# Kernel tuning notes

Measured on AMD Instinct MI355X. Metric: run time of the kernel, lower is better.

## Reference

```python
import jax, jax.numpy as jnp
import numpy as np

B, H, S, DK, DV = 4, 16, 2048, 64, 64

def setup_inputs() -> dict:
    key = jax.random.key(0)
    k1, k2, k3, k4 = jax.random.split(key, 4)
    Q = jax.random.normal(k1, (B, H, S, DK), dtype=jnp.float32)
    K = jax.random.normal(k2, (B, H, S, DK), dtype=jnp.float32)
    V = jax.random.normal(k3, (B, H, S, DV), dtype=jnp.float32)
    mask_out = jax.random.randint(k4, (B, 1, 1, S), 0, 2).astype(jnp.bool_)
    return {"Q": Q, "K": K, "V": V, "mask_out": mask_out}

def reference(Q, K, V, mask_out):
    key_size = Q.shape[-1]
    seq_q, seq_k = Q.shape[-2], K.shape[-2]
    scale = jnp.sqrt(jnp.float32(key_size))
    # scores: [B, H, Sq, Sk]
    scores = jnp.einsum('bhqd,bhkd->bhqk', Q, K) / scale
    scores = jnp.where(mask_out, jnp.float32(-1e9), scores)
    attn = jax.nn.softmax(scores, axis=-1)
    # Gaussian relative-position decay: exp(-|i-j|^2 / (Sk^2 / 2))
    idx_q = jnp.arange(seq_q, dtype=jnp.float32)[:, None]
    idx_k = jnp.arange(seq_k, dtype=jnp.float32)[None, :]
    rel = idx_q - idx_k  # [Sq, Sk]
    decay = jnp.exp(-(rel * rel) * (2.0 / (seq_k * seq_k)))  # [Sq, Sk]
    attn = attn * decay  # broadcast over [B, H]
    return jnp.einsum('bhqk,bhkv->bhqv', attn, V)
```

## Files before the change

kernel.cpp:

```cpp
#include <hip/hip_runtime.h>
#include <hip/hip_bf16.h>
#include <hip/hip_fp16.h>

typedef __attribute__((ext_vector_type(8))) short bf16x8;
typedef __attribute__((ext_vector_type(4))) short bf16x4;
typedef __attribute__((ext_vector_type(4))) float f32x4;
typedef __attribute__((ext_vector_type(4))) unsigned u32x4;
typedef __attribute__((ext_vector_type(4))) int i32x4;

constexpr int Bn = 4, Hn = 16, S = 2048, D = 64;
constexpr int BQ = 128;
constexpr float LOG2E = 1.44269504088896340736f;

__device__ __forceinline__ unsigned cvtpk(float lo, float hi) {
    unsigned r;
    asm("v_cvt_pk_bf16_f32 %0, %1, %2" : "=v"(r) : "v"(lo), "v"(hi));
    return r;
}

__device__ __forceinline__ f32x4 mfma16(bf16x4 a, bf16x4 b, f32x4 c) {
#if __has_builtin(__builtin_amdgcn_mfma_f32_16x16x16bf16_1k)
    return __builtin_amdgcn_mfma_f32_16x16x16bf16_1k(a, b, c, 0, 0, 0);
#else
    asm volatile("v_mfma_f32_16x16x16_bf16 %0, %1, %2, %0"
                 : "+v"(c) : "v"(a), "v"(b));
    return c;
#endif
}

__device__ __forceinline__ void gload16(const short* g, short* lds) {
    __builtin_amdgcn_global_load_lds(
        (const __attribute__((address_space(1))) unsigned*)g,
        (__attribute__((address_space(3))) unsigned*)lds,
        16, 0, 0);
}

__global__ void compact_mask(const void* __restrict__ maskg,
                             int* __restrict__ idxp, int* __restrict__ Mg) {
    const int b = blockIdx.x, t = threadIdx.x;
    __shared__ int wsum[4];
    __shared__ int Msh;

    const unsigned* mu = (const unsigned*)maskg;
    bool is_bytes = false;
    #pragma unroll 8
    for (int i = 0; i < 64; ++i) is_bytes |= (mu[i] > 1u);

    int keep[8]; int cnt = 0;
    #pragma unroll
    for (int i = 0; i < 8; ++i) {
        const int key = t * 8 + i;
        int m;
        if (is_bytes) m = ((const unsigned char*)maskg)[b * S + key];
        else          m = ((const int*)maskg)[b * S + key];
        keep[i] = (m == 0);
        cnt += keep[i];
    }
    const int l = t & 63, w = t >> 6;
    int pre = cnt;
    #pragma unroll
    for (int d = 1; d < 64; d <<= 1) {
        int v = __shfl_up(pre, d, 64);
        if (l >= d) pre += v;
    }
    if (l == 63) wsum[w] = pre;
    __syncthreads();
    int base = 0;
    for (int i = 0; i < w; ++i) base += wsum[i];
    int offs = base + pre - cnt;
    #pragma unroll
    for (int i = 0; i < 8; ++i)
        if (keep[i]) idxp[b * S + (offs++)] = t * 8 + i;
    if (t == 255) Msh = base + pre;
    __syncthreads();
    const int M = Msh;
    for (int i = M + t; i < S; i += 256) idxp[b * S + i] = 0;
    if (M == 0)
        for (int i = t; i < S; i += 256) idxp[b * S + i] = i;
    if (t == 0) Mg[b] = (M == 0) ? -1 : M;
}

__global__ void pack_kv(const float* __restrict__ Kg, const float* __restrict__ Vg,
                        const int* __restrict__ idxp, const int* __restrict__ Mg,
                        short* __restrict__ Kw, short* __restrict__ Vw) {
    const int bh = blockIdx.x, b = bh >> 4;
    const int ck0 = blockIdx.y * 256;
    const int t = threadIdx.x;
    const int Mraw = Mg[b];
    const int M = (Mraw < 0) ? S : Mraw;
    if (ck0 >= M) return;
    const int* idxb = idxp + b * S;
    const float* Kp = Kg + (size_t)bh * S * D;
    const float* Vp = Vg + (size_t)bh * S * D;

    {
        const int dc = (t & 7) * 8;
        #pragma unroll
        for (int tile = 0; tile < 4; ++tile)
            #pragma unroll
            for (int it = 0; it < 2; ++it) {
                const int key = ck0 + tile * 64 + (t >> 3) + it * 32;
                u32x4 pk = u32x4{0u, 0u, 0u, 0u};
                if (key < M) {
                    const float* src = Kp + (size_t)idxb[key] * D + dc;
                    #pragma unroll
                    for (int jj = 0; jj < 4; ++jj)
                        pk[jj] = cvtpk(src[2 * jj], src[2 * jj + 1]);
                }
                *(u32x4*)(Kw + ((size_t)bh * S + key) * D + dc) = pk;
            }
    }
    {
        const int dv = t & 63;
        const int kb = (t >> 6) * 16;
        #pragma unroll
        for (int tile = 0; tile < 4; ++tile) {
            const int tg = (ck0 >> 6) + tile;
            float f[16];
            #pragma unroll
            for (int i = 0; i < 16; ++i) {
                const int key = ck0 + tile * 64 + kb + i;
                float v = 0.f;
                if (key < M) {
                    int row = idxb[key];
                    row = __builtin_amdgcn_readfirstlane(row);
                    v = Vp[(size_t)row * D + dv];
                }
                f[i] = v;
            }
            u32x4 p0, p1;
            #pragma unroll
            for (int jj = 0; jj < 4; ++jj) {
                p0[jj] = cvtpk(f[2 * jj], f[2 * jj + 1]);
                p1[jj] = cvtpk(f[8 + 2 * jj], f[9 + 2 * jj]);
            }
            short* dst = Vw + (((size_t)bh * 32 + tg) * 64 + dv) * 64 + kb;
            *(u32x4*)dst = p0;
            *(u32x4*)(dst + 8) = p1;
        }
    }
}

template<int MINW>
__global__ __launch_bounds__(512, MINW) void attn_packed(
    const float* __restrict__ Qg, const short* __restrict__ Kw,
    const short* __restrict__ Vw, const int* __restrict__ idxp,
    const int* __restrict__ Mg, float* __restrict__ outg)
{
    __shared__ alignas(16) short Kt[2][64][64];
    __shared__ alignas(16) short Vt[2][64][64];
    __shared__ alignas(16) __half dtab[2176];

    const int bid  = blockIdx.x;
    const int lblk = ((bid & 7) << 7) | (bid >> 3);
    const int qt   = lblk & 15;
    const int bh   = lblk >> 4;
    const int b    = bh >> 4;
    const int q0   = qt * BQ;

    const float* Qp   = Qg + ((size_t)bh * S + q0) * D;
    const short* Ksrc = Kw + (size_t)bh * S * D;
    const short* Vsrc = Vw + (size_t)bh * 32 * 64 * 64;
    float*       Op   = outg + ((size_t)bh * S + q0) * D;
    const int*   idxb = idxp + b * S;

    const int t  = threadIdx.x;
    const int w  = t >> 6;
    const int lr = t & 15;
    const int lg = (t & 63) >> 4;
    const int lx = lr & 7;

    const int  Mraw    = Mg[b];
    const bool uniform = (Mraw < 0);
    const int  M       = uniform ? S : Mraw;
    const int  ntiles  = (M + 63) >> 6;

    const int srcoff = ((t >> 3) << 6) + (((t & 7) ^ ((t >> 3) & 7)) << 3);
    const int wbase  = w << 9;

    gload16(Ksrc + srcoff, &Kt[0][0][0] + wbase);
    gload16(Vsrc + srcoff, &Vt[0][0][0] + wbase);

    const float CD2 = (2.0f / ((float)S * (float)S)) * LOG2E;
    for (int i = t; i < 2176; i += 512) {
        const float r = (float)(q0 + i - 2047);
        dtab[i] = __float2half(__builtin_exp2f(-CD2 * r * r));
    }

    const float qscale = uniform ? 0.0f : 0.125f * LOG2E;
    bf16x8 qf[2];
    {
        const int row = w * 16 + lr;
        #pragma unroll
        for (int g = 0; g < 2; ++g) {
            const float* src = Qp + row * D + g * 32 + lg * 8;
            union { unsigned u[4]; bf16x8 v; } cv;
            #pragma unroll
            for (int jj = 0; jj < 4; ++jj)
                cv.u[jj] = cvtpk(src[2 * jj] * qscale, src[2 * jj + 1] * qscale);
            qf[g] = cv.v;
        }
    }

    f32x4 Oacc[4];
    #pragma unroll
    for (int dt = 0; dt < 4; ++dt) Oacc[dt] = f32x4{0.f, 0.f, 0.f, 0.f};
    float lrun = 0.f;

    const int qi = w * 16 + lr + 2047;

    asm volatile("s_waitcnt vmcnt(0)" ::: "memory");
    __syncthreads();

    int c = 0;
    for (int tt = 0; tt < ntiles; ++tt) {
        const int  rem  = M - tt * 64;
        const bool last = (rem <= 64);

        if (tt + 1 < ntiles) {
            const size_t toff = (size_t)(tt + 1) * 4096 + srcoff;
            gload16(Ksrc + toff, &Kt[c ^ 1][0][0] + wbase);
            gload16(Vsrc + toff, &Vt[c ^ 1][0][0] + wbase);
        }

        const char* kbase = (const char*)&Kt[c][0][0];
        const char* vbase = (const char*)&Vt[c][0][0];

        float lp = 0.f;
        #pragma unroll
        for (int kt = 0; kt < 4; ++kt) {
            const bf16x8 kf0 = *(const bf16x8*)(kbase + (kt * 16 + lr) * 128
                                                + ((lg ^ lx) << 4));
            const bf16x8 kf1 = *(const bf16x8*)(kbase + (kt * 16 + lr) * 128
                                                + (((4 + lg) ^ lx) << 4));
            f32x4 s = f32x4{0.f, 0.f, 0.f, 0.f};
            __builtin_amdgcn_s_setprio(1);
            s = __builtin_amdgcn_mfma_f32_16x16x32_bf16(kf0, qf[0], s, 0, 0, 0);
            s = __builtin_amdgcn_mfma_f32_16x16x32_bf16(kf1, qf[1], s, 0, 0, 0);
            __builtin_amdgcn_s_setprio(0);

            const i32x4 iv = *(const i32x4*)(idxb + tt * 64 + kt * 16 + lg * 4);
            float p0 = __builtin_exp2f(s[0] - 16.0f);
            float p1 = __builtin_exp2f(s[1] - 16.0f);
            float p2 = __builtin_exp2f(s[2] - 16.0f);
            float p3 = __builtin_exp2f(s[3] - 16.0f);
            if (last) {
                const int ck = kt * 16 + lg * 4;
                p0 = (ck + 0 < rem) ? p0 : 0.f;
                p1 = (ck + 1 < rem) ? p1 : 0.f;
                p2 = (ck + 2 < rem) ? p2 : 0.f;
                p3 = (ck + 3 < rem) ? p3 : 0.f;
            }
            lp += (p0 + p1) + (p2 + p3);
            const float d0 = __half2float(dtab[qi - iv[0]]);
            const float d1 = __half2float(dtab[qi - iv[1]]);
            const float d2 = __half2float(dtab[qi - iv[2]]);
            const float d3 = __half2float(dtab[qi - iv[3]]);
            union { unsigned u[2]; bf16x4 v; } cx;
            cx.u[0] = cvtpk(p0 * d0, p1 * d1);
            cx.u[1] = cvtpk(p2 * d2, p3 * d3);
            const bf16x4 Xb = cx.v;

            __builtin_amdgcn_s_setprio(1);
            #pragma unroll
            for (int dt = 0; dt < 4; ++dt) {
                const bf16x4 vA = *(const bf16x4*)(vbase + (dt * 16 + lr) * 128
                          + ((((2 * kt + (lg >> 1)) ^ lx) << 4) | ((lg & 1) << 3)));
                Oacc[dt] = mfma16(vA, Xb, Oacc[dt]);
            }
            __builtin_amdgcn_s_setprio(0);
        }
        lrun += lp;

        asm volatile("s_waitcnt vmcnt(0)" ::: "memory");
        __syncthreads();
        c ^= 1;
    }

    {
        float ls = lrun;
        ls += __shfl_xor(ls, 16, 64);
        ls += __shfl_xor(ls, 32, 64);
        const float inv = 1.0f / ls;
        const int row = w * 16 + lr;
        #pragma unroll
        for (int dt = 0; dt < 4; ++dt) {
            f32x4 o = Oacc[dt];
            o[0] *= inv; o[1] *= inv; o[2] *= inv; o[3] *= inv;
            *(f32x4*)&Op[(size_t)row * D + dt * 16 + lg * 4] = o;
        }
    }
}

__global__ __launch_bounds__(256, 3) void attn_gather(
    const float* __restrict__ Qg, const float* __restrict__ Kg,
    const float* __restrict__ Vg, const int* __restrict__ idxp,
    const int* __restrict__ Mg, float* __restrict__ outg)
{
    __shared__ alignas(16) short Kt[64][72];
    __shared__ alignas(16) short Vt[64][72];
    __shared__ alignas(16) float dtab[2176];
    __shared__ alignas(16) int   idxs[64];

    const int blk = blockIdx.x;
    const int qt  = blk & 15;
    const int bh  = blk >> 4;
    const int b   = bh >> 4;
    const int q0  = qt * BQ;

    const float* Qp = Qg + ((size_t)bh * S + q0) * D;
    const float* Kp = Kg + (size_t)bh * S * D;
    const float* Vp = Vg + (size_t)bh * S * D;
    float*       Op = outg + ((size_t)bh * S + q0) * D;
    const int*   idxb = idxp + b * S;

    const int t  = threadIdx.x;
    const int w  = t >> 6;
    const int l  = t & 63;
    const int lr = l & 15;
    const int lg = l >> 4;

    const int  Mraw    = Mg[b];
    const bool uniform = (Mraw < 0);
    const int  M       = uniform ? S : Mraw;

    const float CD2 = (2.0f / ((float)S * (float)S)) * LOG2E;
    for (int i = t; i < 2176; i += 256) {
        const float r = (float)(q0 + i - 2047);
        dtab[i] = __builtin_exp2f(-CD2 * r * r);
    }

    const float qscale = uniform ? 0.0f : 0.125f * LOG2E;
    bf16x8 qf[2][2];
    #pragma unroll
    for (int rt = 0; rt < 2; ++rt) {
        const int row = w * 32 + rt * 16 + lr;
        #pragma unroll
        for (int g = 0; g < 2; ++g) {
            const float* src = Qp + row * D + g * 32 + lg * 8;
            union { unsigned u[4]; bf16x8 v; } cv;
            #pragma unroll
            for (int jj = 0; jj < 4; ++jj)
                cv.u[jj] = cvtpk(src[2 * jj] * qscale, src[2 * jj + 1] * qscale);
            qf[rt][g] = cv.v;
        }
    }

    f32x4 Oacc[2][4];
    #pragma unroll
    for (int rt = 0; rt < 2; ++rt)
        #pragma unroll
        for (int dt = 0; dt < 4; ++dt) Oacc[rt][dt] = f32x4{0.f, 0.f, 0.f, 0.f};
    float lrun[2] = {0.f, 0.f};

    const int qrl2047 = w * 32 + lr + 2047;

    for (int kv = 0; kv < M; kv += 64) {
        const int  rem  = M - kv;
        const bool last = (rem <= 64);
        __syncthreads();
        {
            const int key = t >> 3;
            const int dc  = (t & 7) * 8;
            #pragma unroll
            for (int it = 0; it < 2; ++it) {
                const int row = idxb[kv + key + it * 32];
                const float* src = Kp + (size_t)row * D + dc;
                u32x4 pk;
                #pragma unroll
                for (int jj = 0; jj < 4; ++jj)
                    pk[jj] = cvtpk(src[2 * jj], src[2 * jj + 1]);
                *(u32x4*)&Kt[key + it * 32][dc] = pk;
            }
        }
        if (t < 64) idxs[t] = idxb[kv + t];
        {
            const int dv = t & 63;
            const int kb = (t >> 6) * 16;
            float f[16];
            #pragma unroll
            for (int i = 0; i < 16; ++i) {
                int row = idxb[kv + kb + i];
                row = __builtin_amdgcn_readfirstlane(row);
                f[i] = Vp[(size_t)row * D + dv];
            }
            u32x4 p0, p1;
            #pragma unroll
            for (int jj = 0; jj < 4; ++jj) {
                p0[jj] = cvtpk(f[2 * jj], f[2 * jj + 1]);
                p1[jj] = cvtpk(f[8 + 2 * jj], f[9 + 2 * jj]);
            }
            *(u32x4*)&Vt[dv][kb]     = p0;
            *(u32x4*)&Vt[dv][kb + 8] = p1;
        }
        __syncthreads();

        bf16x8 kf[4][2];
        #pragma unroll
        for (int kt = 0; kt < 4; ++kt)
            #pragma unroll
            for (int g = 0; g < 2; ++g)
                kf[kt][g] = *(const bf16x8*)&Kt[kt * 16 + lr][g * 32 + lg * 8];

        bf16x4 Xb[2][4];
        #pragma unroll
        for (int rt = 0; rt < 2; ++rt) {
            f32x4 sc[4];
            #pragma unroll
            for (int kt = 0; kt < 4; ++kt) {
                f32x4 acc = f32x4{0.f, 0.f, 0.f, 0.f};
                acc = __builtin_amdgcn_mfma_f32_16x16x32_bf16(kf[kt][0], qf[rt][0], acc, 0, 0, 0);
                acc = __builtin_amdgcn_mfma_f32_16x16x32_bf16(kf[kt][1], qf[rt][1], acc, 0, 0, 0);
                sc[kt] = acc;
            }
            const int qi = qrl2047 + rt * 16;
            float lp = 0.f;
            #pragma unroll
            for (int kt = 0; kt < 4; ++kt) {
                const i32x4 iv = *(const i32x4*)&idxs[kt * 16 + lg * 4];
                float p0 = __builtin_exp2f(sc[kt][0] - 16.0f);
                float p1 = __builtin_exp2f(sc[kt][1] - 16.0f);
                float p2 = __builtin_exp2f(sc[kt][2] - 16.0f);
                float p3 = __builtin_exp2f(sc[kt][3] - 16.0f);
                if (last) {
                    const int ck = kt * 16 + lg * 4;
                    p0 = (ck + 0 < rem) ? p0 : 0.f;
                    p1 = (ck + 1 < rem) ? p1 : 0.f;
                    p2 = (ck + 2 < rem) ? p2 : 0.f;
                    p3 = (ck + 3 < rem) ? p3 : 0.f;
                }
                lp += (p0 + p1) + (p2 + p3);
                const float d0 = dtab[qi - iv[0]];
                const float d1 = dtab[qi - iv[1]];
                const float d2 = dtab[qi - iv[2]];
                const float d3 = dtab[qi - iv[3]];
                union { unsigned u[2]; bf16x4 v; } cx;
                cx.u[0] = cvtpk(p0 * d0, p1 * d1);
                cx.u[1] = cvtpk(p2 * d2, p3 * d3);
                Xb[rt][kt] = cx.v;
            }
            lrun[rt] += lp;
        }

        #pragma unroll
        for (int kt = 0; kt < 4; ++kt) {
            bf16x4 vA[4];
            #pragma unroll
            for (int dt = 0; dt < 4; ++dt)
                vA[dt] = *(const bf16x4*)&Vt[dt * 16 + lr][kt * 16 + lg * 4];
            #pragma unroll
            for (int dt = 0; dt < 4; ++dt) {
                Oacc[0][dt] = mfma16(vA[dt], Xb[0][kt], Oacc[0][dt]);
                Oacc[1][dt] = mfma16(vA[dt], Xb[1][kt], Oacc[1][dt]);
            }
        }
    }

    #pragma unroll
    for (int rt = 0; rt < 2; ++rt) {
        float ls = lrun[rt];
        ls += __shfl_xor(ls, 16, 64);
        ls += __shfl_xor(ls, 32, 64);
        const float inv = 1.0f / ls;
        const int row = w * 32 + rt * 16 + lr;
        #pragma unroll
        for (int dt = 0; dt < 4; ++dt) {
            f32x4 o = Oacc[rt][dt];
            o[0] *= inv; o[1] *= inv; o[2] *= inv; o[3] *= inv;
            *(f32x4*)&Op[(size_t)row * D + dt * 16 + lg * 4] = o;
        }
    }
}

extern "C" void kernel_launch(void* const* d_in, const int* in_sizes, int n_in,
                              void* d_out, int out_size, void* d_ws, size_t ws_size,
                              hipStream_t stream) {
    const float* Q = (const float*)d_in[0];
    const float* K = (const float*)d_in[1];
    const float* V = (const float*)d_in[2];
    const void*  M = d_in[3];
    float* out = (float*)d_out;

    int* idxp = (int*)d_ws;
    int* Mg   = idxp + Bn * S;
    size_t base = (((size_t)(Bn * S + Bn) * 4) + 255) & ~(size_t)255;
    short* Kw = (short*)((char*)d_ws + base);
    short* Vw = Kw + (size_t)Bn * Hn * S * D;
    const size_t need = base + 2 * (size_t)Bn * Hn * S * D * sizeof(short);

    compact_mask<<<dim3(Bn), dim3(256), 0, stream>>>(M, idxp, Mg);
    const int nblk = Bn * Hn * (S / BQ);
    if (ws_size >= need) {
        pack_kv<<<dim3(Bn * Hn, S / 256), dim3(256), 0, stream>>>(K, V, idxp, Mg, Kw, Vw);
        hipFuncAttributes fa8{};
        bool use8 = (hipFuncGetAttributes(&fa8,
                        reinterpret_cast<const void*>(&attn_packed<8>)) == hipSuccess)
                    && (fa8.localSizeBytes == 0);
        if (use8)
            attn_packed<8><<<dim3(nblk), dim3(512), 0, stream>>>(Q, Kw, Vw, idxp, Mg, out);
        else
            attn_packed<4><<<dim3(nblk), dim3(512), 0, stream>>>(Q, Kw, Vw, idxp, Mg, out);
    } else {
        attn_gather<<<dim3(nblk), dim3(256), 0, stream>>>(Q, K, V, idxp, Mg, out);
    }
}
```

Measured before the change: 120.7 us.

## Compute Gaussian decay analytically in exponent and process two row tiles per wave

Replaces the per-block half-precision decay lookup table and per-key index gathers with precomputed per-key exponent coefficients (e, f), so the decay folds into the softmax exp2 argument via an FMA. The coefficients are written by compact_mask and streamed into LDS alongside K/V tiles. The attention kernel drops to 256 threads, with each wave handling 32 query rows (two 16-row tiles) so every K/V LDS fragment is reused across both tiles. This doubles the exp2 count per score (one for the normaliser, one for the decayed weight) and raises register pressure, in exchange for removing the dtab build, the table lookups and the idx loads.

```diff
diff --git a/kernel.cpp b/kernel.cpp
--- a/kernel.cpp
+++ b/kernel.cpp
@@ -1,6 +1,5 @@
 #include <hip/hip_runtime.h>
 #include <hip/hip_bf16.h>
-#include <hip/hip_fp16.h>
 
 typedef __attribute__((ext_vector_type(8))) short bf16x8;
 typedef __attribute__((ext_vector_type(4))) short bf16x4;
@@ -11,6 +10,7 @@
 constexpr int Bn = 4, Hn = 16, S = 2048, D = 64;
 constexpr int BQ = 128;
 constexpr float LOG2E = 1.44269504088896340736f;
+constexpr float CD2f = (2.0f / ((float)S * (float)S)) * LOG2E;
 
 __device__ __forceinline__ unsigned cvtpk(float lo, float hi) {
     unsigned r;
@@ -36,7 +36,8 @@
 }
 
 __global__ void compact_mask(const void* __restrict__ maskg,
-                             int* __restrict__ idxp, int* __restrict__ Mg) {
+                             int* __restrict__ idxp, int* __restrict__ Mg,
+                             float* __restrict__ EFw) {
     const int b = blockIdx.x, t = threadIdx.x;
     __shared__ int wsum[4];
     __shared__ int Msh;
@@ -78,6 +79,19 @@
     if (M == 0)
         for (int i = t; i < S; i += 256) idxp[b * S + i] = i;
     if (t == 0) Mg[b] = (M == 0) ? -1 : M;
+
+    const int Meff = (M == 0) ? S : M;
+    for (int key = t; key < S; key += 256) {
+        float e = 0.f, f = 0.f;
+        if (key < Meff) {
+            const int j = (M == 0) ? key : idxp[b * S + key];
+            const float jf = (float)j;
+            f = 2.0f * CD2f * jf;
+            e = -CD2f * jf * jf;
+        }
+        float* dst = EFw + (size_t)b * 8192 + ((key >> 6) * 256 + (key & 63) * 2);
+        dst[0] = e; dst[1] = f;
+    }
 }
 
 __global__ void pack_kv(const float* __restrict__ Kg, const float* __restrict__ Vg,
@@ -141,15 +155,14 @@
     }
 }
 
-template<int MINW>
-__global__ __launch_bounds__(512, MINW) void attn_packed(
+__global__ __launch_bounds__(256, 4) void attn_packed(
     const float* __restrict__ Qg, const short* __restrict__ Kw,
-    const short* __restrict__ Vw, const int* __restrict__ idxp,
+    const short* __restrict__ Vw, const float* __restrict__ EFw,
     const int* __restrict__ Mg, float* __restrict__ outg)
 {
     __shared__ alignas(16) short Kt[2][64][64];
     __shared__ alignas(16) short Vt[2][64][64];
-    __shared__ alignas(16) __half dtab[2176];
+    __shared__ alignas(16) float EFt[2][256];
 
     const int bid  = blockIdx.x;
     const int lblk = ((bid & 7) << 7) | (bid >> 3);
@@ -158,16 +171,17 @@
     const int b    = bh >> 4;
     const int q0   = qt * BQ;
 
-    const float* Qp   = Qg + ((size_t)bh * S + q0) * D;
-    const short* Ksrc = Kw + (size_t)bh * S * D;
-    const short* Vsrc = Vw + (size_t)bh * 32 * 64 * 64;
-    float*       Op   = outg + ((size_t)bh * S + q0) * D;
-    const int*   idxb = idxp + b * S;
+    const float* Qp    = Qg + ((size_t)bh * S + q0) * D;
+    const short* Ksrc  = Kw + (size_t)bh * S * D;
+    const short* Vsrc  = Vw + (size_t)bh * 32 * 64 * 64;
+    const float* EFsrc = EFw + (size_t)b * 8192;
+    float*       Op    = outg + ((size_t)bh * S + q0) * D;
 
     const int t  = threadIdx.x;
     const int w  = t >> 6;
-    const int lr = t & 15;
-    const int lg = (t & 63) >> 4;
+    const int l  = t & 63;
+    const int lr = l & 15;
+    const int lg = l >> 4;
     const int lx = lr & 7;
 
     const int  Mraw    = Mg[b];
@@ -175,22 +189,28 @@
     const int  M       = uniform ? S : Mraw;
     const int  ntiles  = (M + 63) >> 6;
 
-    const int srcoff = ((t >> 3) << 6) + (((t & 7) ^ ((t >> 3) & 7)) << 3);
-    const int wbase  = w << 9;
-
-    gload16(Ksrc + srcoff, &Kt[0][0][0] + wbase);
-    gload16(Vsrc + srcoff, &Vt[0][0][0] + wbase);
-
-    const float CD2 = (2.0f / ((float)S * (float)S)) * LOG2E;
-    for (int i = t; i < 2176; i += 512) {
-        const float r = (float)(q0 + i - 2047);
-        dtab[i] = __float2half(__builtin_exp2f(-CD2 * r * r));
+    int so[2], ld[2];
+    #pragma unroll
+    for (int p = 0; p < 2; ++p) {
+        const int r = (p * 4 + w) * 8 + (l >> 3);
+        so[p] = r * 64 + (((l & 7) ^ (r & 7)) << 3);
+        ld[p] = (p * 4 + w) * 512;
+    }
+    const short* efl = (const short*)EFsrc + l * 8;
+
+    {
+        gload16(Ksrc + so[0], &Kt[0][0][0] + ld[0]);
+        gload16(Ksrc + so[1], &Kt[0][0][0] + ld[1]);
+        gload16(Vsrc + so[0], &Vt[0][0][0] + ld[0]);
+        gload16(Vsrc + so[1], &Vt[0][0][0] + ld[1]);
+        if (w == 0) gload16(efl, (short*)&EFt[0][0]);
     }
 
     const float qscale = uniform ? 0.0f : 0.125f * LOG2E;
-    bf16x8 qf[2];
-    {
-        const int row = w * 16 + lr;
+    bf16x8 qf[2][2];
+    #pragma unroll
+    for (int rt = 0; rt < 2; ++rt) {
+        const int row = w * 32 + rt * 16 + lr;
         #pragma unroll
         for (int g = 0; g < 2; ++g) {
             const float* src = Qp + row * D + g * 32 + lg * 8;
@@ -198,16 +218,24 @@
             #pragma unroll
             for (int jj = 0; jj < 4; ++jj)
                 cv.u[jj] = cvtpk(src[2 * jj] * qscale, src[2 * jj + 1] * qscale);
-            qf[g] = cv.v;
-        }
-    }
-
-    f32x4 Oacc[4];
-    #pragma unroll
-    for (int dt = 0; dt < 4; ++dt) Oacc[dt] = f32x4{0.f, 0.f, 0.f, 0.f};
-    float lrun = 0.f;
-
-    const int qi = w * 16 + lr + 2047;
+            qf[rt][g] = cv.v;
+        }
+    }
+
+    float if_[2], ci2[2];
+    #pragma unroll
+    for (int rt = 0; rt < 2; ++rt) {
+        const float iq = (float)(q0 + w * 32 + rt * 16 + lr);
+        if_[rt] = iq;
+        ci2[rt] = -CD2f * iq * iq;
+    }
+
+    f32x4 Oacc[2][4];
+    #pragma unroll
+    for (int rt = 0; rt < 2; ++rt)
+        #pragma unroll
+        for (int dt = 0; dt < 4; ++dt) Oacc[rt][dt] = f32x4{0.f, 0.f, 0.f, 0.f};
+    float lrun[2] = {0.f, 0.f};
 
     asm volatile("s_waitcnt vmcnt(0)" ::: "memory");
     __syncthreads();
@@ -218,74 +246,92 @@
         const bool last = (rem <= 64);
 
         if (tt + 1 < ntiles) {
-            const size_t toff = (size_t)(tt + 1) * 4096 + srcoff;
-            gload16(Ksrc + toff, &Kt[c ^ 1][0][0] + wbase);
-            gload16(Vsrc + toff, &Vt[c ^ 1][0][0] + wbase);
-        }
-
-        const char* kbase = (const char*)&Kt[c][0][0];
-        const char* vbase = (const char*)&Vt[c][0][0];
-
-        float lp = 0.f;
+            const short* kp = Ksrc + (size_t)(tt + 1) * 4096;
+            const short* vp = Vsrc + (size_t)(tt + 1) * 4096;
+            gload16(kp + so[0], &Kt[c ^ 1][0][0] + ld[0]);
+            gload16(kp + so[1], &Kt[c ^ 1][0][0] + ld[1]);
+            gload16(vp + so[0], &Vt[c ^ 1][0][0] + ld[0]);
+            gload16(vp + so[1], &Vt[c ^ 1][0][0] + ld[1]);
+            if (w == 0) gload16(efl + (size_t)(tt + 1) * 512, (short*)&EFt[c ^ 1][0]);
+        }
+
+        const char*  kbase = (const char*)&Kt[c][0][0];
+        const char*  vbase = (const char*)&Vt[c][0][0];
+        const float* efb   = &EFt[c][0];
+
         #pragma unroll
         for (int kt = 0; kt < 4; ++kt) {
             const bf16x8 kf0 = *(const bf16x8*)(kbase + (kt * 16 + lr) * 128
                                                 + ((lg ^ lx) << 4));
             const bf16x8 kf1 = *(const bf16x8*)(kbase + (kt * 16 + lr) * 128
                                                 + (((4 + lg) ^ lx) << 4));
-            f32x4 s = f32x4{0.f, 0.f, 0.f, 0.f};
+            f32x4 s0 = f32x4{0.f, 0.f, 0.f, 0.f};
+            f32x4 s1 = f32x4{0.f, 0.f, 0.f, 0.f};
             __builtin_amdgcn_s_setprio(1);
-            s = __builtin_amdgcn_mfma_f32_16x16x32_bf16(kf0, qf[0], s, 0, 0, 0);
-            s = __builtin_amdgcn_mfma_f32_16x16x32_bf16(kf1, qf[1], s, 0, 0, 0);
+            s0 = __builtin_amdgcn_mfma_f32_16x16x32_bf16(kf0, qf[0][0], s0, 0, 0, 0);
+            s0 = __builtin_amdgcn_mfma_f32_16x16x32_bf16(kf1, qf[0][1], s0, 0, 0, 0);
+            s1 = __builtin_amdgcn_mfma_f32_16x16x32_bf16(kf0, qf[1][0], s1, 0, 0, 0);
+            s1 = __builtin_amdgcn_mfma_f32_16x16x32_bf16(kf1, qf[1][1], s1, 0, 0, 0);
             __builtin_amdgcn_s_setprio(0);
 
-            const i32x4 iv = *(const i32x4*)(idxb + tt * 64 + kt * 16 + lg * 4);
-            float p0 = __builtin_exp2f(s[0] - 16.0f);
-            float p1 = __builtin_exp2f(s[1] - 16.0f);
-            float p2 = __builtin_exp2f(s[2] - 16.0f);
-            float p3 = __builtin_exp2f(s[3] - 16.0f);
-            if (last) {
-                const int ck = kt * 16 + lg * 4;
-                p0 = (ck + 0 < rem) ? p0 : 0.f;
-                p1 = (ck + 1 < rem) ? p1 : 0.f;
-                p2 = (ck + 2 < rem) ? p2 : 0.f;
-                p3 = (ck + 3 < rem) ? p3 : 0.f;
-            }
-            lp += (p0 + p1) + (p2 + p3);
-            const float d0 = __half2float(dtab[qi - iv[0]]);
-            const float d1 = __half2float(dtab[qi - iv[1]]);
-            const float d2 = __half2float(dtab[qi - iv[2]]);
-            const float d3 = __half2float(dtab[qi - iv[3]]);
-            union { unsigned u[2]; bf16x4 v; } cx;
-            cx.u[0] = cvtpk(p0 * d0, p1 * d1);
-            cx.u[1] = cvtpk(p2 * d2, p3 * d3);
-            const bf16x4 Xb = cx.v;
+            const f32x4 efA = *(const f32x4*)(efb + (kt * 16 + lg * 4) * 2);
+            const f32x4 efB = *(const f32x4*)(efb + (kt * 16 + lg * 4) * 2 + 4);
+
+            bf16x4 Xb[2];
+            #pragma unroll
+            for (int rt = 0; rt < 2; ++rt) {
+                const f32x4 s = rt ? s1 : s0;
+                const float iq = if_[rt], cc = ci2[rt];
+                const float u0 = fmaf(efA[1], iq, efA[0]) + cc;
+                const float u1 = fmaf(efA[3], iq, efA[2]) + cc;
+                const float u2 = fmaf(efB[1], iq, efB[0]) + cc;
+                const float u3 = fmaf(efB[3], iq, efB[2]) + cc;
+                const float a0 = s[0] - 16.0f, a1 = s[1] - 16.0f;
+                const float a2 = s[2] - 16.0f, a3 = s[3] - 16.0f;
+                float p0 = __builtin_exp2f(a0), q0_ = __builtin_exp2f(a0 + u0);
+                float p1 = __builtin_exp2f(a1), q1_ = __builtin_exp2f(a1 + u1);
+                float p2 = __builtin_exp2f(a2), q2_ = __builtin_exp2f(a2 + u2);
+                float p3 = __builtin_exp2f(a3), q3_ = __builtin_exp2f(a3 + u3);
+                if (last) {
+                    const int ck = kt * 16 + lg * 4;
+                    p0 = (ck + 0 < rem) ? p0 : 0.f;  q0_ = (ck + 0 < rem) ? q0_ : 0.f;
+                    p1 = (ck + 1 < rem) ? p1 : 0.f;  q1_ = (ck + 1 < rem) ? q1_ : 0.f;
+                    p2 = (ck + 2 < rem) ? p2 : 0.f;  q2_ = (ck + 2 < rem) ? q2_ : 0.f;
+                    p3 = (ck + 3 < rem) ? p3 : 0.f;  q3_ = (ck + 3 < rem) ? q3_ : 0.f;
+                }
+                lrun[rt] += (p0 + p1) + (p2 + p3);
+                union { unsigned u[2]; bf16x4 v; } cx;
+                cx.u[0] = cvtpk(q0_, q1_);
+                cx.u[1] = cvtpk(q2_, q3_);
+                Xb[rt] = cx.v;
+            }
 
             __builtin_amdgcn_s_setprio(1);
             #pragma unroll
             for (int dt = 0; dt < 4; ++dt) {
                 const bf16x4 vA = *(const bf16x4*)(vbase + (dt * 16 + lr) * 128
                           + ((((2 * kt + (lg >> 1)) ^ lx) << 4) | ((lg & 1) << 3)));
-                Oacc[dt] = mfma16(vA, Xb, Oacc[dt]);
+                Oacc[0][dt] = mfma16(vA, Xb[0], Oacc[0][dt]);
+                Oacc[1][dt] = mfma16(vA, Xb[1], Oacc[1][dt]);
             }
             __builtin_amdgcn_s_setprio(0);
         }
-        lrun += lp;
 
         asm volatile("s_waitcnt vmcnt(0)" ::: "memory");
         __syncthreads();
         c ^= 1;
     }
 
-    {
-        float ls = lrun;
+    #pragma unroll
+    for (int rt = 0; rt < 2; ++rt) {
+        float ls = lrun[rt];
         ls += __shfl_xor(ls, 16, 64);
         ls += __shfl_xor(ls, 32, 64);
         const float inv = 1.0f / ls;
-        const int row = w * 16 + lr;
+        const int row = w * 32 + rt * 16 + lr;
         #pragma unroll
         for (int dt = 0; dt < 4; ++dt) {
-            f32x4 o = Oacc[dt];
+            f32x4 o = Oacc[rt][dt];
             o[0] *= inv; o[1] *= inv; o[2] *= inv; o[3] *= inv;
             *(f32x4*)&Op[(size_t)row * D + dt * 16 + lg * 4] = o;
         }
@@ -324,10 +370,9 @@
     const bool uniform = (Mraw < 0);
     const int  M       = uniform ? S : Mraw;
 
-    const float CD2 = (2.0f / ((float)S * (float)S)) * LOG2E;
     for (int i = t; i < 2176; i += 256) {
         const float r = (float)(q0 + i - 2047);
-        dtab[i] = __builtin_exp2f(-CD2 * r * r);
+        dtab[i] = __builtin_exp2f(-CD2f * r * r);
     }
 
     const float qscale = uniform ? 0.0f : 0.125f * LOG2E;
@@ -484,22 +529,17 @@
     int* idxp = (int*)d_ws;
     int* Mg   = idxp + Bn * S;
     size_t base = (((size_t)(Bn * S + Bn) * 4) + 255) & ~(size_t)255;
-    short* Kw = (short*)((char*)d_ws + base);
+    float* EFw = (float*)((char*)d_ws + base);
+    size_t base2 = base + (size_t)Bn * 32 * 256 * sizeof(float);
+    short* Kw = (short*)((char*)d_ws + base2);
     short* Vw = Kw + (size_t)Bn * Hn * S * D;
-    const size_t need = base + 2 * (size_t)Bn * Hn * S * D * sizeof(short);
-
-    compact_mask<<<dim3(Bn), dim3(256), 0, stream>>>(M, idxp, Mg);
+    const size_t need = base2 + 2 * (size_t)Bn * Hn * S * D * sizeof(short);
+
+    compact_mask<<<dim3(Bn), dim3(256), 0, stream>>>(M, idxp, Mg, EFw);
     const int nblk = Bn * Hn * (S / BQ);
     if (ws_size >= need) {
         pack_kv<<<dim3(Bn * Hn, S / 256), dim3(256), 0, stream>>>(K, V, idxp, Mg, Kw, Vw);
-        hipFuncAttributes fa8{};
-        bool use8 = (hipFuncGetAttributes(&fa8,
-                        reinterpret_cast<const void*>(&attn_packed<8>)) == hipSuccess)
-                    && (fa8.localSizeBytes == 0);
-        if (use8)
-            attn_packed<8><<<dim3(nblk), dim3(512), 0, stream>>>(Q, Kw, Vw, idxp, Mg, out);
-        else
-            attn_packed<4><<<dim3(nblk), dim3(512), 0, stream>>>(Q, Kw, Vw, idxp, Mg, out);
+        attn_packed<<<dim3(nblk), dim3(256), 0, stream>>>(Q, Kw, Vw, EFw, Mg, out);
     } else {
         attn_gather<<<dim3(nblk), dim3(256), 0, stream>>>(Q, K, V, idxp, Mg, out);
     }
```

Result: slower. 149.6 us (+23.9%).
